# Performance work log

Hardware: AMD Instinct MI355X
Metric: run time of the kernel (lower is better)

Reference implementation:

```python
import jax, jax.numpy as jnp
import numpy as np

DIM = 192
HEADS = 8
EPS = 1e-12  # torch F.normalize eps


def setup_inputs() -> dict:
    key = jax.random.key(0)
    ks = jax.random.split(key, 6)
    b, c, h, w = 8, DIM, 128, 128
    x = jax.random.normal(ks[0], (b, c, h, w), dtype=jnp.float32)
    feature = jax.random.normal(ks[1], (b, c, h, w), dtype=jnp.float32)
    # Conv2d(dim, 3*dim, 1, bias=False) -> weight (3*dim, dim, 1, 1); store squeezed (3*dim, dim)
    W_qkv = jax.random.normal(ks[2], (3 * c, c), dtype=jnp.float32) * (1.0 / np.sqrt(c))
    # Depthwise Conv2d(3*dim, 3*dim, 3, padding=1, groups=3*dim) -> weight (3*dim, 1, 3, 3)
    W_dw = jax.random.normal(ks[3], (3 * c, 1, 3, 3), dtype=jnp.float32) * (1.0 / 3.0)
    # Conv2d(dim, dim, 1, bias=False) -> (dim, dim)
    W_proj = jax.random.normal(ks[4], (c, c), dtype=jnp.float32) * (1.0 / np.sqrt(c))
    temperature = jnp.ones((HEADS, 1, 1), dtype=jnp.float32)
    return {"x": x, "feature": feature, "W_qkv": W_qkv, "W_dw": W_dw,
            "W_proj": W_proj, "temperature": temperature}


def _l2_normalize(t):
    # torch F.normalize(dim=-1): t / max(||t||_2, eps)
    n = jnp.sqrt(jnp.sum(t * t, axis=-1, keepdims=True))
    return t / jnp.maximum(n, EPS)


def reference(x, feature, W_qkv, W_dw, W_proj, temperature):
    b, c, h, w = x.shape
    head = HEADS
    ch = c // head  # channels per head
    # 1x1 conv (pointwise): bchw,oc -> bohw
    qkv = jnp.einsum('bchw,oc->bohw', x, W_qkv)
    # 3x3 depthwise conv, padding=1
    qkv = jax.lax.conv_general_dilated(
        qkv, W_dw, window_strides=(1, 1), padding=((1, 1), (1, 1)),
        dimension_numbers=('NCHW', 'OIHW', 'NCHW'), feature_group_count=3 * c)
    q, k, v = jnp.split(qkv, 3, axis=1)
    # b (head ch) h w -> b head ch (h w)
    q = q.reshape(b, head, ch, h * w)
    k = k.reshape(b, head, ch, h * w)
    v = v.reshape(b, head, ch, h * w)
    f = feature.reshape(b, head, ch, h * w)
    q = _l2_normalize(q * f)
    k = _l2_normalize(k * f)
    # small c x c attention per (batch, head)
    attn = jnp.einsum('bhcn,bhdn->bhcd', q, k) * temperature
    attn = jax.nn.softmax(attn, axis=-1)
    out = jnp.einsum('bhcd,bhdn->bhcn', attn, v)
    out = out.reshape(b, c, h, w)
    out = jnp.einsum('bchw,oc->bohw', out, W_proj)
    return out
```

## Files before the change

kernel.cpp:

```cpp
#include <hip/hip_runtime.h>

typedef unsigned short u16;
typedef short s16x8 __attribute__((ext_vector_type(8)));
typedef float f32x4 __attribute__((ext_vector_type(4)));

__device__ __forceinline__ float bf2f(u16 u) {
  return __uint_as_float(((unsigned)u) << 16);
}
__device__ __forceinline__ u16 f2bf(float f) {
  unsigned x = __float_as_uint(f);
  return (u16)((x + 0x7fffu + ((x >> 16) & 1u)) >> 16);
}

template<bool IN_FP32>
__global__ __launch_bounds__(256) void transpose_k(
    const void* __restrict__ inp, u16* __restrict__ outp,
    long batchStride, int chanOffset)
{
  __shared__ float lds[64][33];
  const int c0 = blockIdx.x * 64, p0 = blockIdx.y * 32, b = blockIdx.z;
  const int t = threadIdx.x;
  {
    const int r = t >> 3, pq = (t & 7) * 4;
    #pragma unroll
    for (int i = 0; i < 2; i++) {
      const int c = r + i * 32;
      const long base = (long)b * batchStride + (long)(chanOffset + c0 + c) * 16384 + p0 + pq;
      if (IN_FP32) {
        const float4 v = *(const float4*)((const float*)inp + base);
        lds[c][pq+0] = v.x; lds[c][pq+1] = v.y; lds[c][pq+2] = v.z; lds[c][pq+3] = v.w;
      } else {
        const u16* s = (const u16*)inp + base;
        lds[c][pq+0] = bf2f(s[0]); lds[c][pq+1] = bf2f(s[1]);
        lds[c][pq+2] = bf2f(s[2]); lds[c][pq+3] = bf2f(s[3]);
      }
    }
  }
  __syncthreads();
  const int p = t >> 3, c8 = (t & 7) * 8;
  union { s16x8 v; u16 u[8]; } pk;
  #pragma unroll
  for (int j = 0; j < 8; j++) pk.u[j] = f2bf(lds[c8 + j][p]);
  *(s16x8*)(outp + ((long)b * 16384 + p0 + p) * 192 + c0 + c8) = pk.v;
}

template<bool A_FP32, bool OUT_BF16>
__global__ __launch_bounds__(256) void gemm_nt(
    const void* __restrict__ Ap, const u16* __restrict__ B,
    void* __restrict__ outp, int mTiles, long aBatchStride)
{
  __shared__ char smem[57344];
  char* const Bs = smem;
  char* const As = smem + 49152;

  const int t = threadIdx.x;
  const int n0 = blockIdx.x * 128;
  const int b  = n0 >> 14;
  const int p0 = n0 & 16383;
  const int wave = t >> 6, lane = t & 63;
  const int l15 = lane & 15, l4 = lane >> 4;

  {
    const uint4* src = (const uint4*)(B + (long)n0 * 192);
    #pragma unroll
    for (int i = 0; i < 12; i++) {
      const int ci = t + i*256;
      const int r = ci / 24, cb = ci % 24;
      const uint4 v = src[ci];
      *(uint4*)(Bs + r*384 + ((cb ^ (r&7)) << 4)) = v;
    }
  }

  const int M = mTiles * 64;
  for (int mt = 0; mt < mTiles; mt++) {
    const int m0 = mt * 64;
    f32x4 acc[4][2];
    #pragma unroll
    for (int i = 0; i < 4; i++)
      #pragma unroll
      for (int j = 0; j < 2; j++) acc[i][j] = (f32x4){0.f, 0.f, 0.f, 0.f};

    for (int kc3 = 0; kc3 < 3; kc3++) {
      if (mt | kc3) __syncthreads();
      #pragma unroll
      for (int i = 0; i < 2; i++) {
        const int ci = t + i*256;
        const int r = ci >> 3, cb = ci & 7;
        union { uint4 v; u16 u[8]; } pk;
        if (A_FP32) {
          const float* src = (const float*)Ap + (long)(m0 + r) * 192 + kc3*64 + cb*8;
          const float4 f0 = ((const float4*)src)[0];
          const float4 f1 = ((const float4*)src)[1];
          pk.u[0]=f2bf(f0.x); pk.u[1]=f2bf(f0.y); pk.u[2]=f2bf(f0.z); pk.u[3]=f2bf(f0.w);
          pk.u[4]=f2bf(f1.x); pk.u[5]=f2bf(f1.y); pk.u[6]=f2bf(f1.z); pk.u[7]=f2bf(f1.w);
        } else {
          pk.v = *(const uint4*)((const u16*)Ap + (long)b * aBatchStride
                                 + (long)(m0 + r) * 192 + kc3*64 + cb*8);
        }
        *(uint4*)(As + r*128 + ((cb ^ (r&7)) << 4)) = pk.v;
      }
      __syncthreads();
      #pragma unroll
      for (int kq = 0; kq < 2; kq++) {
        const int kbA = kq*4 + l4;
        const int kbB = kc3*8 + kq*4 + l4;
        s16x8 af[4], bfr[2];
        #pragma unroll
        for (int mi = 0; mi < 4; mi++) {
          const int row = mi*16 + l15;
          af[mi] = *(const s16x8*)(As + row*128 + ((kbA ^ (row&7)) << 4));
        }
        #pragma unroll
        for (int ni = 0; ni < 2; ni++) {
          const int row = wave*32 + ni*16 + l15;
          bfr[ni] = *(const s16x8*)(Bs + row*384 + ((kbB ^ (row&7)) << 4));
        }
        #pragma unroll
        for (int mi = 0; mi < 4; mi++)
          #pragma unroll
          for (int ni = 0; ni < 2; ni++)
            acc[mi][ni] = __builtin_amdgcn_mfma_f32_16x16x32_bf16(af[mi], bfr[ni], acc[mi][ni], 0, 0, 0);
      }
    }
    const long outBase = (long)b * M * 16384;
    #pragma unroll
    for (int mi = 0; mi < 4; mi++) {
      #pragma unroll
      for (int ni = 0; ni < 2; ni++) {
        const int col = p0 + wave*32 + ni*16 + l15;
        #pragma unroll
        for (int j = 0; j < 4; j++) {
          const int row = m0 + mi*16 + l4*4 + j;
          const float v = acc[mi][ni][j];
          if (OUT_BF16) ((u16*)outp)[outBase + (long)row * 16384 + col] = f2bf(v);
          else          ((float*)outp)[outBase + (long)row * 16384 + col] = v;
        }
      }
    }
  }
}

__global__ __launch_bounds__(256) void dwconv_k(
    u16* __restrict__ qkv, const float* __restrict__ Wdw)
{
  __shared__ u16 lds[130*132];
  const int ch = blockIdx.x, b = blockIdx.y;
  u16* const base = qkv + ((long)b * 576 + ch) * 16384;
  const int t = threadIdx.x;

  {
    uint4* z = (uint4*)lds;
    #pragma unroll
    for (int i = 0; i < 9; i++) {
      const int idx = t + i*256;
      if (idx < 2145) z[idx] = (uint4){0,0,0,0};
    }
  }
  float w[9];
  #pragma unroll
  for (int i = 0; i < 9; i++) w[i] = Wdw[ch*9 + i];
  __syncthreads();

  #pragma unroll
  for (int i = 0; i < 8; i++) {
    const int p = t + i*256;
    const int y = p >> 4, x = (p & 15) * 8;
    union { uint4 v; u16 u[8]; } ld;
    ld.v = *(const uint4*)(base + y*128 + x);
    u16* d = &lds[(y+1)*132 + x + 1];
    #pragma unroll
    for (int k = 0; k < 8; k++) d[k] = ld.u[k];
  }
  __syncthreads();

  #pragma unroll
  for (int i = 0; i < 8; i++) {
    const int p = t + i*256;
    const int y = p >> 4, x = (p & 15) * 8;
    float r[3][10];
    #pragma unroll
    for (int dy = 0; dy < 3; dy++)
      #pragma unroll
      for (int j = 0; j < 10; j++)
        r[dy][j] = bf2f(lds[(y+dy)*132 + x + j]);
    float acc[8];
    #pragma unroll
    for (int xx = 0; xx < 8; xx++)
      acc[xx] = w[0]*r[0][xx] + w[1]*r[0][xx+1] + w[2]*r[0][xx+2]
              + w[3]*r[1][xx] + w[4]*r[1][xx+1] + w[5]*r[1][xx+2]
              + w[6]*r[2][xx] + w[7]*r[2][xx+1] + w[8]*r[2][xx+2];
    union { uint4 v; u16 u[8]; } st;
    #pragma unroll
    for (int xx = 0; xx < 8; xx++) st.u[xx] = f2bf(acc[xx]);
    *(uint4*)(base + y*128 + x) = st.v;
  }
}

__global__ __launch_bounds__(256) void gram_k(
    const u16* __restrict__ qkv, const float* __restrict__ feature,
    float* __restrict__ Gp)
{
  __shared__ u16 us[48*128];
  __shared__ float red[4*2304];
  const int kc = blockIdx.x, bh = blockIdx.y;
  const int b = bh >> 3, h = bh & 7;
  const int t = threadIdx.x, wave = t >> 6, lane = t & 63;
  const int l15 = lane & 15, l4 = lane >> 4;
  const u16* const qbase = qkv + ((long)b*576 + h*24) * 16384;
  const u16* const kbase = qkv + ((long)b*576 + 192 + h*24) * 16384;
  const float* const fbase = feature + ((long)b*192 + h*24) * 16384;
  char* const usb = (char*)us;

  f32x4 acc[3][3];
  #pragma unroll
  for (int i = 0; i < 3; i++)
    #pragma unroll
    for (int j = 0; j < 3; j++) acc[i][j] = (f32x4){0.f, 0.f, 0.f, 0.f};

  for (int step = 0; step < 16; step++) {
    const int k0 = kc*2048 + step*128;
    #pragma unroll
    for (int i = 0; i < 3; i++) {
      const int idx = t + i*256;
      const int r = idx >> 5, d4 = idx & 31;
      const long po = (long)r*16384 + k0 + d4*4;
      const float4 f4 = *(const float4*)(fbase + po);
      union { uint2 v; u16 u[4]; } uq, uk, oq, ok;
      uq.v = *(const uint2*)(qbase + po);
      uk.v = *(const uint2*)(kbase + po);
      const float fv[4] = {f4.x, f4.y, f4.z, f4.w};
      #pragma unroll
      for (int j = 0; j < 4; j++) {
        oq.u[j] = f2bf(bf2f(uq.u[j]) * fv[j]);
        ok.u[j] = f2bf(bf2f(uk.u[j]) * fv[j]);
      }
      const int col = d4*4;
      const int sub = ((col&7)<<1);
      const int r2 = r + 24;
      *(uint2*)(usb + r *256 + (((col>>3) ^ (r &7)) << 4) + sub) = oq.v;
      *(uint2*)(usb + r2*256 + (((col>>3) ^ (r2&7)) << 4) + sub) = ok.v;
    }
    __syncthreads();
    {
      const int kb = wave*4 + l4;
      s16x8 fr[3];
      #pragma unroll
      for (int g = 0; g < 3; g++) {
        const int row = g*16 + l15;
        fr[g] = *(const s16x8*)(usb + row*256 + ((kb ^ (row&7)) << 4));
      }
      #pragma unroll
      for (int gm = 0; gm < 3; gm++)
        #pragma unroll
        for (int gn = 0; gn < 3; gn++)
          acc[gm][gn] = __builtin_amdgcn_mfma_f32_16x16x32_bf16(fr[gm], fr[gn], acc[gm][gn], 0, 0, 0);
    }
    __syncthreads();
  }
  #pragma unroll
  for (int gm = 0; gm < 3; gm++)
    #pragma unroll
    for (int gn = 0; gn < 3; gn++)
      #pragma unroll
      for (int j = 0; j < 4; j++) {
        const int r = gm*16 + l4*4 + j, s = gn*16 + l15;
        red[wave*2304 + r*48 + s] = acc[gm][gn][j];
      }
  __syncthreads();
  for (int idx = t; idx < 2304; idx += 256) {
    const float sum = red[idx] + red[2304+idx] + red[4608+idx] + red[6912+idx];
    Gp[((long)bh*8 + kc)*2304 + idx] = sum;
  }
}

__global__ __launch_bounds__(256) void attnfin_k(
    const float* __restrict__ Gp, const float* __restrict__ temperature,
    float* __restrict__ attn)
{
  __shared__ float cross[576];
  __shared__ float qn[24], kn[24];
  const int bh = blockIdx.x, h = bh & 7;
  const int t = threadIdx.x;
  const float* const g = Gp + (long)bh * 8 * 2304;
  for (int idx = t; idx < 624; idx += 256) {
    float s = 0.f;
    if (idx < 576) {
      const int c = idx / 24, d = idx - c * 24;
      #pragma unroll
      for (int kc = 0; kc < 8; kc++) s += g[kc*2304 + c*48 + 24 + d];
      cross[idx] = s;
    } else {
      const int r = idx - 576;
      #pragma unroll
      for (int kc = 0; kc < 8; kc++) s += g[kc*2304 + r*48 + r];
      const float nv = fmaxf(sqrtf(s), 1e-12f);
      if (r < 24) qn[r] = nv; else kn[r-24] = nv;
    }
  }
  __syncthreads();
  if (t < 24) {
    const float tmp = temperature[h];
    const float qi = 1.f / qn[t];
    float vals[24];
    float m = -1e30f;
    #pragma unroll
    for (int d = 0; d < 24; d++) {
      const float v = cross[t*24 + d] * qi / kn[d] * tmp;
      vals[d] = v; m = fmaxf(m, v);
    }
    float s = 0.f;
    #pragma unroll
    for (int d = 0; d < 24; d++) { vals[d] = __expf(vals[d] - m); s += vals[d]; }
    const float inv = 1.f / s;
    #pragma unroll
    for (int d = 0; d < 24; d++) attn[(long)bh*576 + t*24 + d] = vals[d] * inv;
  }
}

__global__ __launch_bounds__(256) void m2_k(
    const float* __restrict__ attn, const float* __restrict__ Wp,
    u16* __restrict__ M2)
{
  const int gid = blockIdx.x * 256 + threadIdx.x;
  const int g = gid % 192;
  const int rem = gid / 192;
  const int o = rem % 192;
  const int b = rem / 192;
  const int h = g / 24, d = g - h*24;
  const float* a = attn + ((long)(b*8 + h) * 24) * 24 + d;
  const float* w = Wp + (long)o * 192 + h * 24;
  float s = 0.f;
  #pragma unroll
  for (int c = 0; c < 24; c++) s += w[c] * a[c*24];
  M2[gid] = f2bf(s);
}

extern "C" void kernel_launch(void* const* d_in, const int* in_sizes, int n_in,
                              void* d_out, int out_size, void* d_ws, size_t ws_size,
                              hipStream_t stream) {
  const float* x    = (const float*)d_in[0];
  const float* fe   = (const float*)d_in[1];
  const float* Wqkv = (const float*)d_in[2];
  const float* Wdw  = (const float*)d_in[3];
  const float* Wpr  = (const float*)d_in[4];
  const float* temp = (const float*)d_in[5];

  char* ws = (char*)d_ws;
  u16*   xT  = (u16*)ws;
  u16*   vT  = xT;
  u16*   qkv = (u16*)(ws + 50331648L);
  float* Gp  = (float*)(ws + 201326592L);
  float* attn= (float*)(ws + 206045184L);
  u16*   M2  = (u16*)(ws + 206192640L);

  transpose_k<true ><<<dim3(3,512,8), 256, 0, stream>>>(x,   xT, 192L*16384, 0);
  gemm_nt<true, true ><<<1024, 256, 0, stream>>>(Wqkv, xT, qkv, 9, 0);
  dwconv_k<<<dim3(576,8), 256, 0, stream>>>(qkv, Wdw);
  transpose_k<false><<<dim3(3,512,8), 256, 0, stream>>>(qkv, vT, 576L*16384, 384);
  gram_k<<<dim3(8,64), 256, 0, stream>>>(qkv, fe, Gp);
  attnfin_k<<<64, 256, 0, stream>>>(Gp, temp, attn);
  m2_k<<<1152, 256, 0, stream>>>(attn, Wpr, M2);
  gemm_nt<false, false><<<1024, 256, 0, stream>>>(M2, vT, d_out, 3, 36864L);
}
```

Before: 280.1 us.

## Split GEMM M-tiles across blocks with XCD-aware mapping and LDS-staged stores

The pointwise GEMMs now launch one block per (N-tile, M-tile) pair instead of looping over all M-tiles in each block. The block index is remapped so that consecutive blocks on the same XCD share an N-tile, which should let the B tile be reused through that XCD's cache. B is loaded per k-chunk into a smaller LDS buffer, cutting shared memory per block and raising occupancy. The output goes through LDS so each thread writes one contiguous vector instead of scattered scalar stores. The cost is that each B tile is fetched from global memory once per M-tile rather than once per block, and the epilogue adds extra barriers.

```diff
diff --git a/kernel.cpp b/kernel.cpp
--- a/kernel.cpp
+++ b/kernel.cpp
@@ -44,98 +44,114 @@
   *(s16x8*)(outp + ((long)b * 16384 + p0 + p) * 192 + c0 + c8) = pk.v;
 }
 
-template<bool A_FP32, bool OUT_BF16>
+template<bool A_FP32, bool OUT_BF16, int MT>
 __global__ __launch_bounds__(256) void gemm_nt(
     const void* __restrict__ Ap, const u16* __restrict__ B,
-    void* __restrict__ outp, int mTiles, long aBatchStride)
-{
-  __shared__ char smem[57344];
-  char* const Bs = smem;
-  char* const As = smem + 49152;
+    void* __restrict__ outp, long aBatchStride)
+{
+  __shared__ char smem[24576];
+  char* const As = smem;
+  char* const Bs = smem + 8192;
+  float* const ldsF = (float*)smem;
 
   const int t = threadIdx.x;
-  const int n0 = blockIdx.x * 128;
+  {
+  }
+  const int i = blockIdx.x;
+  const int xcd = i & 7, kk = i >> 3;
+  const int n  = xcd + 8 * (kk / MT);
+  const int m0 = (kk % MT) * 64;
+  const int n0 = n * 128;
   const int b  = n0 >> 14;
   const int p0 = n0 & 16383;
   const int wave = t >> 6, lane = t & 63;
   const int l15 = lane & 15, l4 = lane >> 4;
 
-  {
-    const uint4* src = (const uint4*)(B + (long)n0 * 192);
-    #pragma unroll
-    for (int i = 0; i < 12; i++) {
-      const int ci = t + i*256;
-      const int r = ci / 24, cb = ci % 24;
-      const uint4 v = src[ci];
-      *(uint4*)(Bs + r*384 + ((cb ^ (r&7)) << 4)) = v;
-    }
-  }
-
-  const int M = mTiles * 64;
-  for (int mt = 0; mt < mTiles; mt++) {
-    const int m0 = mt * 64;
-    f32x4 acc[4][2];
-    #pragma unroll
-    for (int i = 0; i < 4; i++)
-      #pragma unroll
-      for (int j = 0; j < 2; j++) acc[i][j] = (f32x4){0.f, 0.f, 0.f, 0.f};
-
-    for (int kc3 = 0; kc3 < 3; kc3++) {
-      if (mt | kc3) __syncthreads();
-      #pragma unroll
-      for (int i = 0; i < 2; i++) {
-        const int ci = t + i*256;
-        const int r = ci >> 3, cb = ci & 7;
-        union { uint4 v; u16 u[8]; } pk;
-        if (A_FP32) {
-          const float* src = (const float*)Ap + (long)(m0 + r) * 192 + kc3*64 + cb*8;
-          const float4 f0 = ((const float4*)src)[0];
-          const float4 f1 = ((const float4*)src)[1];
-          pk.u[0]=f2bf(f0.x); pk.u[1]=f2bf(f0.y); pk.u[2]=f2bf(f0.z); pk.u[3]=f2bf(f0.w);
-          pk.u[4]=f2bf(f1.x); pk.u[5]=f2bf(f1.y); pk.u[6]=f2bf(f1.z); pk.u[7]=f2bf(f1.w);
-        } else {
-          pk.v = *(const uint4*)((const u16*)Ap + (long)b * aBatchStride
-                                 + (long)(m0 + r) * 192 + kc3*64 + cb*8);
-        }
-        *(uint4*)(As + r*128 + ((cb ^ (r&7)) << 4)) = pk.v;
-      }
-      __syncthreads();
-      #pragma unroll
-      for (int kq = 0; kq < 2; kq++) {
-        const int kbA = kq*4 + l4;
-        const int kbB = kc3*8 + kq*4 + l4;
-        s16x8 af[4], bfr[2];
+  f32x4 acc[4][2];
+  #pragma unroll
+  for (int ii = 0; ii < 4; ii++)
+    #pragma unroll
+    for (int j = 0; j < 2; j++) acc[ii][j] = (f32x4){0.f, 0.f, 0.f, 0.f};
+
+  const u16* const Bbase = B + (long)n0 * 192;
+  const int ar = t >> 2, ac0 = (t & 3) * 16;
+  const int br = t >> 1, bc0 = (t & 1) * 32;
+
+  for (int kc = 0; kc < 192; kc += 64) {
+    if (kc) __syncthreads();
+    if (A_FP32) {
+      const float* src = (const float*)Ap + (long)(m0 + ar) * 192 + kc + ac0;
+      #pragma unroll
+      for (int ii = 0; ii < 2; ii++) {
+        float4 f0 = ((const float4*)src)[2*ii];
+        float4 f1 = ((const float4*)src)[2*ii+1];
+        union { s16x8 v; u16 u[8]; } pk;
+        pk.u[0]=f2bf(f0.x); pk.u[1]=f2bf(f0.y); pk.u[2]=f2bf(f0.z); pk.u[3]=f2bf(f0.w);
+        pk.u[4]=f2bf(f1.x); pk.u[5]=f2bf(f1.y); pk.u[6]=f2bf(f1.z); pk.u[7]=f2bf(f1.w);
+        *(s16x8*)(As + ar*128 + ((((ac0>>3)+ii) ^ (ar&7)) << 4)) = pk.v;
+      }
+    } else {
+      const u16* src = (const u16*)Ap + (long)b * aBatchStride + (long)(m0 + ar) * 192 + kc + ac0;
+      #pragma unroll
+      for (int ii = 0; ii < 2; ii++) {
+        s16x8 v = *(const s16x8*)(src + ii*8);
+        *(s16x8*)(As + ar*128 + ((((ac0>>3)+ii) ^ (ar&7)) << 4)) = v;
+      }
+    }
+    {
+      const u16* src = Bbase + (long)br * 192 + kc + bc0;
+      #pragma unroll
+      for (int ii = 0; ii < 4; ii++) {
+        s16x8 v = *(const s16x8*)(src + ii*8);
+        *(s16x8*)(Bs + br*128 + ((((bc0>>3)+ii) ^ (br&7)) << 4)) = v;
+      }
+    }
+    __syncthreads();
+    #pragma unroll
+    for (int kq = 0; kq < 2; kq++) {
+      const int kb = kq*4 + l4;
+      s16x8 af[4], bfr[2];
+      #pragma unroll
+      for (int mi = 0; mi < 4; mi++) {
+        const int row = mi*16 + l15;
+        af[mi] = *(const s16x8*)(As + row*128 + ((kb ^ (row&7)) << 4));
+      }
+      #pragma unroll
+      for (int ni = 0; ni < 2; ni++) {
+        const int row = wave*32 + ni*16 + l15;
+        bfr[ni] = *(const s16x8*)(Bs + row*128 + ((kb ^ (row&7)) << 4));
+      }
+      #pragma unroll
+      for (int mi = 0; mi < 4; mi++)
         #pragma unroll
-        for (int mi = 0; mi < 4; mi++) {
-          const int row = mi*16 + l15;
-          af[mi] = *(const s16x8*)(As + row*128 + ((kbA ^ (row&7)) << 4));
-        }
-        #pragma unroll
-        for (int ni = 0; ni < 2; ni++) {
-          const int row = wave*32 + ni*16 + l15;
-          bfr[ni] = *(const s16x8*)(Bs + row*384 + ((kbB ^ (row&7)) << 4));
-        }
-        #pragma unroll
-        for (int mi = 0; mi < 4; mi++)
-          #pragma unroll
-          for (int ni = 0; ni < 2; ni++)
-            acc[mi][ni] = __builtin_amdgcn_mfma_f32_16x16x32_bf16(af[mi], bfr[ni], acc[mi][ni], 0, 0, 0);
-      }
-    }
-    const long outBase = (long)b * M * 16384;
-    #pragma unroll
-    for (int mi = 0; mi < 4; mi++) {
-      #pragma unroll
-      for (int ni = 0; ni < 2; ni++) {
-        const int col = p0 + wave*32 + ni*16 + l15;
-        #pragma unroll
-        for (int j = 0; j < 4; j++) {
-          const int row = m0 + mi*16 + l4*4 + j;
-          const float v = acc[mi][ni][j];
-          if (OUT_BF16) ((u16*)outp)[outBase + (long)row * 16384 + col] = f2bf(v);
-          else          ((float*)outp)[outBase + (long)row * 16384 + col] = v;
-        }
-      }
+        for (int ni = 0; ni < 2; ni++)
+          acc[mi][ni] = __builtin_amdgcn_mfma_f32_16x16x32_bf16(af[mi], bfr[ni], acc[mi][ni], 0, 0, 0);
+    }
+  }
+
+  const long outBase = (long)b * (MT*64) * 16384;
+  #pragma unroll
+  for (int mi = 0; mi < 4; mi++) {
+    __syncthreads();
+    #pragma unroll
+    for (int ni = 0; ni < 2; ni++)
+      #pragma unroll
+      for (int j = 0; j < 4; j++)
+        ldsF[(l4*4 + j)*132 + wave*32 + ni*16 + l15] = acc[mi][ni][j];
+    __syncthreads();
+    const int r = t >> 4, c8 = (t & 15) * 8;
+    const float* src = &ldsF[r*132 + c8];
+    const long gaddr = outBase + (long)(m0 + mi*16 + r) * 16384 + p0 + c8;
+    if (OUT_BF16) {
+      union { uint4 v; u16 u[8]; } pk;
+      #pragma unroll
+      for (int jj = 0; jj < 8; jj++) pk.u[jj] = f2bf(src[jj]);
+      *(uint4*)((u16*)outp + gaddr) = pk.v;
+    } else {
+      const float4 a0 = *(const float4*)(src);
+      const float4 a1 = *(const float4*)(src + 4);
+      *(float4*)((float*)outp + gaddr) = a0;
+      *(float4*)((float*)outp + gaddr + 4) = a1;
     }
   }
 }
@@ -354,11 +370,11 @@
   u16*   M2  = (u16*)(ws + 206192640L);
 
   transpose_k<true ><<<dim3(3,512,8), 256, 0, stream>>>(x,   xT, 192L*16384, 0);
-  gemm_nt<true, true ><<<1024, 256, 0, stream>>>(Wqkv, xT, qkv, 9, 0);
+  gemm_nt<true, true, 9><<<9216, 256, 0, stream>>>(Wqkv, xT, qkv, 0);
   dwconv_k<<<dim3(576,8), 256, 0, stream>>>(qkv, Wdw);
   transpose_k<false><<<dim3(3,512,8), 256, 0, stream>>>(qkv, vT, 576L*16384, 384);
   gram_k<<<dim3(8,64), 256, 0, stream>>>(qkv, fe, Gp);
   attnfin_k<<<64, 256, 0, stream>>>(Gp, temp, attn);
   m2_k<<<1152, 256, 0, stream>>>(attn, Wpr, M2);
-  gemm_nt<false, false><<<1024, 256, 0, stream>>>(M2, vT, d_out, 3, 36864L);
-}
+  gemm_nt<false, false, 3><<<3072, 256, 0, stream>>>(M2, vT, d_out, 36864L);
+}
```

Result: no change. 283.4 us (+1.2%).

## Replace LDS-staged GEMM with register-resident A tile and double-buffered B loads

Applied to the files above, without the earlier changes.

The GEMM kernel no longer stages operands through shared memory. Each block keeps a full 64x192 slice of the weight matrix in registers and streams several 128-column B tiles straight from global memory, double-buffered in registers. Blocks are remapped so that neighbouring M tiles of the same column chunk land on the same XCD, which should improve L2 reuse of B. This removes the LDS traffic and the barriers, at the cost of higher register pressure (a launch-bounds occupancy hint of 2) and uncoalesced direct-fragment global loads.

```diff
diff --git a/kernel.cpp b/kernel.cpp
--- a/kernel.cpp
+++ b/kernel.cpp
@@ -44,90 +44,86 @@
   *(s16x8*)(outp + ((long)b * 16384 + p0 + p) * 192 + c0 + c8) = pk.v;
 }
 
-template<bool A_FP32, bool OUT_BF16>
-__global__ __launch_bounds__(256) void gemm_nt(
-    const void* __restrict__ Ap, const u16* __restrict__ B,
-    void* __restrict__ outp, int mTiles, long aBatchStride)
-{
-  __shared__ char smem[57344];
-  char* const Bs = smem;
-  char* const As = smem + 49152;
-
+template<bool A_FP32, bool OUT_BF16, int MT, int NTILES>
+__global__ __launch_bounds__(256, 2) void gemm_areg(
+    const void* __restrict__ Ap, const u16* __restrict__ Bp,
+    void* __restrict__ outp, long aBatchStride)
+{
   const int t = threadIdx.x;
-  const int n0 = blockIdx.x * 128;
-  const int b  = n0 >> 14;
-  const int p0 = n0 & 16383;
   const int wave = t >> 6, lane = t & 63;
   const int l15 = lane & 15, l4 = lane >> 4;
 
-  {
-    const uint4* src = (const uint4*)(B + (long)n0 * 192);
-    #pragma unroll
-    for (int i = 0; i < 12; i++) {
-      const int ci = t + i*256;
-      const int r = ci / 24, cb = ci % 24;
-      const uint4 v = src[ci];
-      *(uint4*)(Bs + r*384 + ((cb ^ (r&7)) << 4)) = v;
-    }
-  }
-
-  const int M = mTiles * 64;
-  for (int mt = 0; mt < mTiles; mt++) {
-    const int m0 = mt * 64;
+  const int i = blockIdx.x;
+  const int xcd = i & 7, k = i >> 3;
+  const int chunk = xcd + 8 * (k / MT);
+  const int m0 = (k % MT) * 64;
+  const int nt0 = chunk * NTILES;
+  const long col0 = (long)nt0 * 128;
+  const int b = (int)(col0 >> 14);
+  const int p0 = (int)(col0 & 16383);
+
+  s16x8 af[4][6];
+  #pragma unroll
+  for (int mi = 0; mi < 4; mi++) {
+    const int row = m0 + mi*16 + l15;
+    #pragma unroll
+    for (int kq = 0; kq < 6; kq++) {
+      const int kc = kq*32 + l4*8;
+      if (A_FP32) {
+        const float* s = (const float*)Ap + (long)row*192 + kc;
+        const float4 f0 = ((const float4*)s)[0];
+        const float4 f1 = ((const float4*)s)[1];
+        union { s16x8 v; u16 u[8]; } pk;
+        pk.u[0]=f2bf(f0.x); pk.u[1]=f2bf(f0.y); pk.u[2]=f2bf(f0.z); pk.u[3]=f2bf(f0.w);
+        pk.u[4]=f2bf(f1.x); pk.u[5]=f2bf(f1.y); pk.u[6]=f2bf(f1.z); pk.u[7]=f2bf(f1.w);
+        af[mi][kq] = pk.v;
+      } else {
+        af[mi][kq] = *(const s16x8*)((const u16*)Ap + (long)b*aBatchStride
+                                     + (long)row*192 + kc);
+      }
+    }
+  }
+
+  auto loadB = [&](s16x8 (&bf)[2][6], int nt) {
+    const long base = ((long)nt*128 + wave*32 + l15) * 192 + l4*8;
+    #pragma unroll
+    for (int ni = 0; ni < 2; ni++)
+      #pragma unroll
+      for (int kq = 0; kq < 6; kq++)
+        bf[ni][kq] = *(const s16x8*)(Bp + base + ni*16*192 + kq*32);
+  };
+
+  s16x8 bA[2][6], bB[2][6];
+  loadB(bA, nt0);
+
+  const long outBase = (long)b * (MT*64) * 16384;
+  #pragma unroll
+  for (int it = 0; it < NTILES; it++) {
+    s16x8 (&bc)[2][6] = (it & 1) ? bB : bA;
+    s16x8 (&bn)[2][6] = (it & 1) ? bA : bB;
+    if (it + 1 < NTILES) loadB(bn, nt0 + it + 1);
+
     f32x4 acc[4][2];
     #pragma unroll
-    for (int i = 0; i < 4; i++)
-      #pragma unroll
-      for (int j = 0; j < 2; j++) acc[i][j] = (f32x4){0.f, 0.f, 0.f, 0.f};
-
-    for (int kc3 = 0; kc3 < 3; kc3++) {
-      if (mt | kc3) __syncthreads();
-      #pragma unroll
-      for (int i = 0; i < 2; i++) {
-        const int ci = t + i*256;
-        const int r = ci >> 3, cb = ci & 7;
-        union { uint4 v; u16 u[8]; } pk;
-        if (A_FP32) {
-          const float* src = (const float*)Ap + (long)(m0 + r) * 192 + kc3*64 + cb*8;
-          const float4 f0 = ((const float4*)src)[0];
-          const float4 f1 = ((const float4*)src)[1];
-          pk.u[0]=f2bf(f0.x); pk.u[1]=f2bf(f0.y); pk.u[2]=f2bf(f0.z); pk.u[3]=f2bf(f0.w);
-          pk.u[4]=f2bf(f1.x); pk.u[5]=f2bf(f1.y); pk.u[6]=f2bf(f1.z); pk.u[7]=f2bf(f1.w);
-        } else {
-          pk.v = *(const uint4*)((const u16*)Ap + (long)b * aBatchStride
-                                 + (long)(m0 + r) * 192 + kc3*64 + cb*8);
-        }
-        *(uint4*)(As + r*128 + ((cb ^ (r&7)) << 4)) = pk.v;
-      }
-      __syncthreads();
-      #pragma unroll
-      for (int kq = 0; kq < 2; kq++) {
-        const int kbA = kq*4 + l4;
-        const int kbB = kc3*8 + kq*4 + l4;
-        s16x8 af[4], bfr[2];
+    for (int mi = 0; mi < 4; mi++)
+      #pragma unroll
+      for (int ni = 0; ni < 2; ni++) acc[mi][ni] = (f32x4){0.f,0.f,0.f,0.f};
+
+    #pragma unroll
+    for (int kq = 0; kq < 6; kq++)
+      #pragma unroll
+      for (int mi = 0; mi < 4; mi++)
         #pragma unroll
-        for (int mi = 0; mi < 4; mi++) {
-          const int row = mi*16 + l15;
-          af[mi] = *(const s16x8*)(As + row*128 + ((kbA ^ (row&7)) << 4));
-        }
-        #pragma unroll
-        for (int ni = 0; ni < 2; ni++) {
-          const int row = wave*32 + ni*16 + l15;
-          bfr[ni] = *(const s16x8*)(Bs + row*384 + ((kbB ^ (row&7)) << 4));
-        }
-        #pragma unroll
-        for (int mi = 0; mi < 4; mi++)
-          #pragma unroll
-          for (int ni = 0; ni < 2; ni++)
-            acc[mi][ni] = __builtin_amdgcn_mfma_f32_16x16x32_bf16(af[mi], bfr[ni], acc[mi][ni], 0, 0, 0);
-      }
-    }
-    const long outBase = (long)b * M * 16384;
+        for (int ni = 0; ni < 2; ni++)
+          acc[mi][ni] = __builtin_amdgcn_mfma_f32_16x16x32_bf16(
+              af[mi][kq], bc[ni][kq], acc[mi][ni], 0, 0, 0);
+
+    const int pt = p0 + it*128 + wave*32;
     #pragma unroll
     for (int mi = 0; mi < 4; mi++) {
       #pragma unroll
       for (int ni = 0; ni < 2; ni++) {
-        const int col = p0 + wave*32 + ni*16 + l15;
+        const int col = pt + ni*16 + l15;
         #pragma unroll
         for (int j = 0; j < 4; j++) {
           const int row = m0 + mi*16 + l4*4 + j;
@@ -169,7 +165,7 @@
     ld.v = *(const uint4*)(base + y*128 + x);
     u16* d = &lds[(y+1)*132 + x + 1];
     #pragma unroll
-    for (int k = 0; k < 8; k++) d[k] = ld.u[k];
+    for (int kk = 0; kk < 8; kk++) d[kk] = ld.u[kk];
   }
   __syncthreads();
 
@@ -354,11 +350,11 @@
   u16*   M2  = (u16*)(ws + 206192640L);
 
   transpose_k<true ><<<dim3(3,512,8), 256, 0, stream>>>(x,   xT, 192L*16384, 0);
-  gemm_nt<true, true ><<<1024, 256, 0, stream>>>(Wqkv, xT, qkv, 9, 0);
+  gemm_areg<true, true, 9, 8><<<1152, 256, 0, stream>>>(Wqkv, xT, qkv, 0);
   dwconv_k<<<dim3(576,8), 256, 0, stream>>>(qkv, Wdw);
   transpose_k<false><<<dim3(3,512,8), 256, 0, stream>>>(qkv, vT, 576L*16384, 384);
   gram_k<<<dim3(8,64), 256, 0, stream>>>(qkv, fe, Gp);
   attnfin_k<<<64, 256, 0, stream>>>(Gp, temp, attn);
   m2_k<<<1152, 256, 0, stream>>>(attn, Wpr, M2);
-  gemm_nt<false, false><<<1024, 256, 0, stream>>>(M2, vT, d_out, 3, 36864L);
-}
+  gemm_areg<false, false, 3, 4><<<768, 256, 0, stream>>>(M2, vT, d_out, 36864L);
+}
```

Result: slower. 309.4 us (+10.5%).
